# Kernel tuning notes

Measured on AMD Instinct MI355X. Metric: run time of the kernel, lower is better.

Reference implementation:

```python
import jax, jax.numpy as jnp
import numpy as np

K = 8          # num groups / object slots
FC = 256       # fc_size
LAST = 128     # last_fc_size
B = 2048       # batch
M = 1024       # input size
H = 512        # state (hidden) size


def _ln(x, g, b):
    # LayerNorm over last dim, eps matches torch default 1e-5
    mu = jnp.mean(x, axis=-1, keepdims=True)
    var = jnp.mean((x - mu) ** 2, axis=-1, keepdims=True)
    return (x - mu) * jax.lax.rsqrt(var + 1e-5) * g + b


def setup_inputs() -> dict:
    key = jax.random.key(0)
    ks = jax.random.split(key, 10)
    s = 0.05
    d = {
        "x": jax.random.normal(ks[0], (B * K, M), jnp.float32),
        "state": jax.random.normal(ks[1], (B * K, H), jnp.float32),
        # encoder: Linear(H->FC) + LN(FC)
        "enc_w": jax.random.normal(ks[2], (H, FC), jnp.float32) * s,
        "enc_b": jnp.zeros((FC,), jnp.float32),
        "enc_g": jnp.ones((FC,), jnp.float32),
        "enc_bb": jnp.zeros((FC,), jnp.float32),
        # core: Linear(2*FC->FC) + LN(FC)
        "core_w": jax.random.normal(ks[3], (2 * FC, FC), jnp.float32) * s,
        "core_b": jnp.zeros((FC,), jnp.float32),
        "core_g": jnp.ones((FC,), jnp.float32),
        "core_bb": jnp.zeros((FC,), jnp.float32),
        # context: Linear(FC->FC) + LN(FC)
        "ctx_w": jax.random.normal(ks[4], (FC, FC), jnp.float32) * s,
        "ctx_b": jnp.zeros((FC,), jnp.float32),
        "ctx_g": jnp.ones((FC,), jnp.float32),
        "ctx_bb": jnp.zeros((FC,), jnp.float32),
        # attention: Linear(FC->LAST) + LN(LAST) + Tanh + Linear(LAST->1) + Sigmoid
        "att1_w": jax.random.normal(ks[5], (FC, LAST), jnp.float32) * s,
        "att1_b": jnp.zeros((LAST,), jnp.float32),
        "att_g": jnp.ones((LAST,), jnp.float32),
        "att_bb": jnp.zeros((LAST,), jnp.float32),
        "att2_w": jax.random.normal(ks[6], (LAST, 1), jnp.float32) * s,
        "att2_b": jnp.zeros((1,), jnp.float32),
        # out_fc: Linear(FC + FC + M -> FC)
        "out_w": jax.random.normal(ks[7], (FC + FC + M, FC), jnp.float32) * s,
        "out_b": jnp.zeros((FC,), jnp.float32),
    }
    return d


def reference(x, state, enc_w, enc_b, enc_g, enc_bb,
              core_w, core_b, core_g, core_bb,
              ctx_w, ctx_b, ctx_g, ctx_bb,
              att1_w, att1_b, att_g, att_bb, att2_w, att2_b,
              out_w, out_b):
    bk, m = x.shape
    k = K
    b = bk // k
    # 0. encode state: [B*K, H] -> [B*K, FC]
    s1 = jax.nn.relu(_ln(state @ enc_w + enc_b, enc_g, enc_bb))
    h1 = s1.shape[-1]
    s1r = s1.reshape(b, k, h1)
    # focus: K-1 copies of each slot's state  [b, k, k-1, h1]
    fs = jnp.broadcast_to(s1r[:, :, None, :], (b, k, k - 1, h1))
    # context: gather the K-1 other slots' states (replaces torch python loop)
    idx = np.array([[j for j in range(k) if j != i] for i in range(k)])  # [k, k-1]
    cs = s1r[:, idx, :]  # [b, k, k-1, h1]
    concat = jnp.concatenate([fs, cs], axis=-1).reshape(b * k * (k - 1), 2 * h1)
    # core / context MLPs over pairs
    core = jax.nn.relu(_ln(concat @ core_w + core_b, core_g, core_bb))   # [b*k*(k-1), FC]
    ctx = jax.nn.relu(_ln(core @ ctx_w + ctx_b, ctx_g, ctx_bb))          # [b*k*(k-1), FC]
    # attention scalar per pair
    att_h = jnp.tanh(_ln(core @ att1_w + att1_b, att_g, att_bb))
    att = jax.nn.sigmoid(att_h @ att2_w + att2_b)                        # [b*k*(k-1), 1]
    # attention-weighted sum over the K-1 context dim
    h2 = ctx.shape[-1]
    effect = jnp.sum(ctx.reshape(b * k, k - 1, h2) * att.reshape(b * k, k - 1, 1), axis=1)
    # decode: concat encoded state, effect, input -> new state
    total = jnp.concatenate([s1, effect, x], axis=-1)
    new_state = total @ out_w + out_b
    return (new_state, new_state)
```

## Files before the change

kernel.cpp:

```cpp
#include <hip/hip_runtime.h>
#include <stdint.h>

#define FC    256
#define HH    512
#define MX    1024
#define LASTN 128
#define NROW  16384
#define NGRP  2048

typedef unsigned short u16;
typedef __bf16 bf16x8 __attribute__((ext_vector_type(8)));
typedef float  f32x4  __attribute__((ext_vector_type(4)));

__device__ __forceinline__ float red16(float v) {
#pragma unroll
  for (int m = 1; m < 16; m <<= 1) v += __shfl_xor(v, m);
  return v;
}
__device__ __forceinline__ float red16hi(float v) {
#pragma unroll
  for (int m = 4; m < 64; m <<= 1) v += __shfl_xor(v, m);
  return v;
}
__device__ __forceinline__ u16 to_bf16(float f) {
  unsigned u = __float_as_uint(f);
  return (u16)((u + 0x8000u) >> 16);
}
__device__ __forceinline__ float from_bf16(u16 s) {
  return __uint_as_float(((unsigned)s) << 16);
}
__device__ __forceinline__ uint32_t pk2(float a, float b) {
  return (uint32_t)to_bf16(a) | ((uint32_t)to_bf16(b) << 16);
}
__device__ __forceinline__ float tanh_fast(float x) {
  float e = __expf(2.f * x);
  return __fdividef(e - 1.f, e + 1.f);
}
__device__ __forceinline__ float sigmoid_fast(float x) {
  return __fdividef(1.f, 1.f + __expf(-x));
}
__device__ __forceinline__ void glds16(const void* g, void* l) {
  __builtin_amdgcn_global_load_lds(
      (__attribute__((address_space(1))) uint32_t*)g,
      (__attribute__((address_space(3))) uint32_t*)l, 16, 0, 0);
}
__device__ __forceinline__ bf16x8 frag_ld(const u16* p) {
  return __builtin_bit_cast(bf16x8, *(const uint4*)p);
}

__global__ __launch_bounds__(256) void k_prep(
    const float* __restrict__ enc_w, const float* __restrict__ core_w,
    const float* __restrict__ ctx_w, const float* __restrict__ att1_w,
    const float* __restrict__ out_w,
    u16* __restrict__ encT, u16* __restrict__ uvT, u16* __restrict__ ctxT,
    u16* __restrict__ attT, u16* __restrict__ outT)
{
  const int bx = blockIdx.x, tid = threadIdx.x;
  const float* W; u16* D; int NKC, N, local; int uv = 0;
  if (bx < 64)       { W = enc_w;  D = encT; NKC = 16; N = 256; local = bx * 256 + tid; }
  else if (bx < 128) { W = core_w; D = uvT;  NKC = 8;  N = 256; local = (bx-64)*256 + tid; uv = 1; }
  else if (bx < 160) { W = ctx_w;  D = ctxT; NKC = 8;  N = 256; local = (bx-128)*256 + tid; }
  else if (bx < 176) { W = att1_w; D = attT; NKC = 8;  N = 128; local = (bx-160)*256 + tid; }
  else               { W = out_w;  D = outT; NKC = 48; N = 256; local = (bx-176)*256 + tid; }
  const int l  = local & 63;
  const int kc = (local >> 6) % NKC;
  const int u  = (local >> 6) / NKC;
  const int n  = u * 16 + (l & 15);
  const int k0 = kc * 32 + (l >> 4) * 8;
  float f[8];
#pragma unroll
  for (int j = 0; j < 8; ++j) {
    const int k = k0 + j;
    if (uv) f[j] = (n < 256) ? W[(size_t)k * 256 + n] : W[(size_t)(256 + k) * 256 + (n - 256)];
    else    f[j] = W[(size_t)k * N + n];
  }
  uint4 w;
  w.x = pk2(f[0], f[1]); w.y = pk2(f[2], f[3]);
  w.z = pk2(f[4], f[5]); w.w = pk2(f[6], f[7]);
  *(uint4*)&D[(size_t)local * 8] = w;
}

__global__ __launch_bounds__(256) void k_enc(
    const float* __restrict__ state, const u16* __restrict__ encT,
    const float* __restrict__ enc_b, const float* __restrict__ enc_g,
    const float* __restrict__ enc_bb, u16* __restrict__ s1b)
{
  __shared__ __align__(16) u16 smA[2][128 * 8];
  __shared__ __align__(16) u16 smB[2][16 * 64 * 8];
  __shared__ float smP[2][2][16][2];
  const int tid = threadIdx.x, wv = tid >> 6, lane = tid & 63;
  const int cl = lane & 15, quad = lane >> 4;
  const int rb = wv >> 1, cb = wv & 1;
  const int row0 = blockIdx.x * 32;
  f32x4 acc[8];
#pragma unroll
  for (int u = 0; u < 8; ++u) acc[u] = (f32x4){0.f, 0.f, 0.f, 0.f};

  for (int kk = 0; kk < 8; ++kk) {
    __syncthreads();
    {
      const int p = tid >> 7, lu = tid & 127;
      const int kc = kk * 2 + p;
      const int rblk = lu >> 6, ll = lu & 63;
      const float* src = state + (size_t)(row0 + rblk * 16 + (ll & 15)) * HH + kc * 32 + (ll >> 4) * 8;
      float4 a = *(const float4*)src, b = *(const float4*)(src + 4);
      uint4 w; w.x = pk2(a.x, a.y); w.y = pk2(a.z, a.w); w.z = pk2(b.x, b.y); w.w = pk2(b.z, b.w);
      *(uint4*)&smA[p][(size_t)lu * 8] = w;
    }
#pragma unroll
    for (int p = 0; p < 2; ++p)
#pragma unroll
      for (int i = 0; i < 4; ++i) {
        const int u = wv * 4 + i;
        glds16(encT + ((size_t)(u * 16 + kk * 2 + p) * 64 + lane) * 8, &smB[p][u * 512]);
      }
    __syncthreads();
#pragma unroll
    for (int p = 0; p < 2; ++p) {
      bf16x8 af = frag_ld(&smA[p][(rb * 64 + lane) * 8]);
#pragma unroll
      for (int u = 0; u < 8; ++u) {
        bf16x8 bf = frag_ld(&smB[p][((cb * 8 + u) * 64 + lane) * 8]);
        acc[u] = __builtin_amdgcn_mfma_f32_16x16x32_bf16(af, bf, acc[u], 0, 0, 0);
      }
    }
  }
  float bias[8], gg[8], bb[8];
#pragma unroll
  for (int u = 0; u < 8; ++u) {
    const int col = cb * 128 + u * 16 + cl;
    bias[u] = enc_b[col]; gg[u] = enc_g[col]; bb[u] = enc_bb[col];
  }
  float vv[4][8];
#pragma unroll
  for (int r4 = 0; r4 < 4; ++r4) {
    float s = 0.f, sq = 0.f;
#pragma unroll
    for (int u = 0; u < 8; ++u) {
      float v = acc[u][r4] + bias[u];
      vv[r4][u] = v; s += v; sq += v * v;
    }
    s = red16(s); sq = red16(sq);
    if (cl == 0) { smP[cb][rb][quad * 4 + r4][0] = s; smP[cb][rb][quad * 4 + r4][1] = sq; }
  }
  __syncthreads();
#pragma unroll
  for (int r4 = 0; r4 < 4; ++r4) {
    const int rr = quad * 4 + r4;
    const float S  = smP[0][rb][rr][0] + smP[1][rb][rr][0];
    const float SQ = smP[0][rb][rr][1] + smP[1][rb][rr][1];
    const float mu = S * (1.f / 256.f);
    const float rs = rsqrtf(SQ * (1.f / 256.f) - mu * mu + 1e-5f);
    const int row = row0 + rb * 16 + rr;
#pragma unroll
    for (int u = 0; u < 8; ++u) {
      float o = fmaxf((vv[r4][u] - mu) * rs * gg[u] + bb[u], 0.f);
      s1b[(size_t)row * FC + cb * 128 + u * 16 + cl] = to_bf16(o);
    }
  }
}

__global__ __launch_bounds__(256) void k_uv(
    const u16* __restrict__ s1b, const u16* __restrict__ uvT,
    float* __restrict__ UV)
{
  __shared__ __align__(16) u16 smA[2][4 * 64 * 8];
  __shared__ __align__(16) u16 smB[2][8 * 64 * 8];
  const int tid = threadIdx.x, wv = tid >> 6, lane = tid & 63;
  const int cl = lane & 15, quad = lane >> 4;
  const int row0 = blockIdx.x * 64;
  const int nb = blockIdx.y;
  f32x4 acc[8];
#pragma unroll
  for (int u = 0; u < 8; ++u) acc[u] = (f32x4){0.f, 0.f, 0.f, 0.f};

  for (int kk = 0; kk < 4; ++kk) {
    __syncthreads();
#pragma unroll
    for (int p = 0; p < 2; ++p) {
      const int kc = kk * 2 + p;
      glds16(s1b + (size_t)(row0 + wv * 16 + (lane & 15)) * FC + kc * 32 + (lane >> 4) * 8,
             &smA[p][wv * 512]);
#pragma unroll
      for (int i = 0; i < 2; ++i) {
        const int u = wv * 2 + i;
        glds16(uvT + ((size_t)((nb * 8 + u) * 8 + kc) * 64 + lane) * 8, &smB[p][u * 512]);
      }
    }
    __syncthreads();
#pragma unroll
    for (int p = 0; p < 2; ++p) {
      bf16x8 af = frag_ld(&smA[p][(wv * 64 + lane) * 8]);
#pragma unroll
      for (int u = 0; u < 8; ++u) {
        bf16x8 bf = frag_ld(&smB[p][(u * 64 + lane) * 8]);
        acc[u] = __builtin_amdgcn_mfma_f32_16x16x32_bf16(af, bf, acc[u], 0, 0, 0);
      }
    }
  }
#pragma unroll
  for (int r4 = 0; r4 < 4; ++r4) {
    const int row = row0 + wv * 16 + quad * 4 + r4;
#pragma unroll
    for (int u = 0; u < 8; ++u)
      UV[(size_t)row * 512 + nb * 128 + u * 16 + cl] = acc[u][r4];
  }
}

__global__ __launch_bounds__(256, 3) void k_pair(
    const float* __restrict__ UV, const float* __restrict__ core_b,
    const float* __restrict__ core_g, const float* __restrict__ core_bb,
    const u16* __restrict__ ctxT, const float* __restrict__ ctx_b,
    const float* __restrict__ ctx_g, const float* __restrict__ ctx_bb,
    const u16* __restrict__ attT, const float* __restrict__ att1_b,
    const float* __restrict__ att_g, const float* __restrict__ att_bb,
    const float* __restrict__ att2_w, const float* __restrict__ att2_b,
    u16* __restrict__ effb)
{
  __shared__ __align__(16) u16 smA[2048 * 8];
  __shared__ __align__(16) u16 smX[16 * 64 * 8];
  __shared__ float att_s[64];
  float* smUV = (float*)smX;
  u16*   smB  = smX;
  const int g = blockIdx.x;
  const int tid = threadIdx.x, wv = tid >> 6, lane = tid & 63;
  const int cl = lane & 15, quad = lane >> 4;
  const int aswz = ((lane >> 5) & 1) << 2;

#pragma unroll
  for (int i = 0; i < 4; ++i) {
    const int r = wv * 4 + i;
    const int row = g * 8 + (r & 7);
    const int half = r >> 3;
    glds16(UV + (size_t)row * 512 + half * 256 + lane * 4, &smUV[r * 256]);
  }
#pragma unroll
  for (int i = 0; i < 8; ++i)
    *(uint4*)&smA[(size_t)(tid + i * 256) * 8] = (uint4){0u, 0u, 0u, 0u};
  __syncthreads();

  {
    const int s4  = lane & 3;
    const int g16 = lane >> 2;
    const int c0  = g16 * 16;
    float4 CB[4], CG[4], CBB[4];
#pragma unroll
    for (int q = 0; q < 4; ++q) {
      const int cq = c0 + ((q ^ s4) << 2);
      CB[q]  = *(const float4*)&core_b[cq];
      CG[q]  = *(const float4*)&core_g[cq];
      CBB[q] = *(const float4*)&core_bb[cq];
    }
#pragma unroll
    for (int it = 0; it < 4; ++it) {
      const int p = it * 16 + wv * 4 + s4;
      if (p < 56) {
        const int i = p / 7, t = p - i * 7;
        const int j = t + (t >= i ? 1 : 0);
        const float* uA = &smUV[i * 256 + c0];
        const float* vB = &smUV[(8 + j) * 256 + c0];
        float v[16];
        float s = 0.f, sq = 0.f;
#pragma unroll
        for (int q = 0; q < 4; ++q) {
          const int qo = (q ^ s4) << 2;
          float4 ua = *(const float4*)(uA + qo);
          float4 vb = *(const float4*)(vB + qo);
          float x0 = ua.x + vb.x + CB[q].x, x1 = ua.y + vb.y + CB[q].y;
          float x2 = ua.z + vb.z + CB[q].z, x3 = ua.w + vb.w + CB[q].w;
          v[q*4+0] = x0; v[q*4+1] = x1; v[q*4+2] = x2; v[q*4+3] = x3;
          s += x0 + x1 + x2 + x3;
          sq += x0*x0 + x1*x1 + x2*x2 + x3*x3;
        }
        s = red16hi(s); sq = red16hi(sq);
        const float mu = s * (1.f / 256.f);
        const float rs = rsqrtf(sq * (1.f / 256.f) - mu * mu + 1e-5f);
#pragma unroll
        for (int q = 0; q < 4; ++q) {
          v[q*4+0] = fmaxf((v[q*4+0] - mu) * rs * CG[q].x + CBB[q].x, 0.f);
          v[q*4+1] = fmaxf((v[q*4+1] - mu) * rs * CG[q].y + CBB[q].y, 0.f);
          v[q*4+2] = fmaxf((v[q*4+2] - mu) * rs * CG[q].z + CBB[q].z, 0.f);
          v[q*4+3] = fmaxf((v[q*4+3] - mu) * rs * CG[q].w + CBB[q].w, 0.f);
        }
#pragma unroll
        for (int q = 0; q < 4; ++q) {
          const int lg = q ^ s4;
          const int ks = (g16 * 2 + (lg >> 1)) & 3;
          int slot = ((p >> 4) * 8 + (g16 >> 1)) * 64 + (p & 15) + 16 * ks;
          slot ^= ((slot >> 5) & 1) << 2;
          uint2 w;
          w.x = pk2(v[q*4+0], v[q*4+1]);
          w.y = pk2(v[q*4+2], v[q*4+3]);
          *(uint2*)&smA[(size_t)slot * 8 + (lg & 1) * 4] = w;
        }
      }
    }
  }
  __syncthreads();

  f32x4 accT[8];
#pragma unroll
  for (int t = 0; t < 8; ++t) accT[t] = (f32x4){0.f, 0.f, 0.f, 0.f};
#pragma unroll 2
  for (int kc = 0; kc < 8; ++kc) {
    uint4 attf[8];
#pragma unroll
    for (int q = 0; q < 8; ++q)
      attf[q] = *(const uint4*)(attT + ((size_t)(q * 8 + kc) * 64 + lane) * 8);
    bf16x8 af = frag_ld(&smA[(size_t)((((wv * 8 + kc) * 64) + lane) ^ aswz) * 8]);
#pragma unroll
    for (int q = 0; q < 8; ++q) {
      bf16x8 bf = __builtin_bit_cast(bf16x8, attf[q]);
      accT[q] = __builtin_amdgcn_mfma_f32_16x16x32_bf16(af, bf, accT[q], 0, 0, 0);
    }
  }

  {
    float ab[8], ag[8], abb[8], aw[8];
#pragma unroll
    for (int t = 0; t < 8; ++t) {
      const int col = t * 16 + cl;
      ab[t] = att1_b[col]; ag[t] = att_g[col]; abb[t] = att_bb[col]; aw[t] = att2_w[col];
    }
    const float b2 = att2_b[0];
#pragma unroll
    for (int r4 = 0; r4 < 4; ++r4) {
      float v[8], s = 0.f, sq = 0.f;
#pragma unroll
      for (int t = 0; t < 8; ++t) {
        v[t] = accT[t][r4] + ab[t];
        s += v[t]; sq += v[t] * v[t];
      }
      s = red16(s); sq = red16(sq);
      const float mu = s * (1.f / 128.f);
      const float rs = rsqrtf(sq * (1.f / 128.f) - mu * mu + 1e-5f);
      float d = 0.f;
#pragma unroll
      for (int t = 0; t < 8; ++t) {
        float h = tanh_fast((v[t] - mu) * rs * ag[t] + abb[t]);
        d = fmaf(h, aw[t], d);
      }
      d = red16(d);
      if (cl == 0) {
        const int r = wv * 16 + quad * 4 + r4;
        if (r < 56) att_s[r] = sigmoid_fast(d + b2);
      }
    }
  }

  f32x4 accC[16];
#pragma unroll
  for (int t = 0; t < 16; ++t) accC[t] = (f32x4){0.f, 0.f, 0.f, 0.f};
  for (int kc = 0; kc < 8; ++kc) {
    if (kc) __syncthreads();
#pragma unroll
    for (int i = 0; i < 4; ++i) {
      const int q = wv * 4 + i;
      glds16(ctxT + ((size_t)(q * 8 + kc) * 64 + lane) * 8, &smB[q * 512]);
    }
    __syncthreads();
    bf16x8 af = frag_ld(&smA[(size_t)((((wv * 8 + kc) * 64) + lane) ^ aswz) * 8]);
#pragma unroll
    for (int q = 0; q < 16; ++q) {
      bf16x8 bf = frag_ld(&smB[(q * 64 + lane) * 8]);
      accC[q] = __builtin_amdgcn_mfma_f32_16x16x32_bf16(af, bf, accC[q], 0, 0, 0);
    }
  }
  __syncthreads();

  u16* smS = smA;
  {
    float cb[16], cg[16], cbb[16];
#pragma unroll
    for (int t = 0; t < 16; ++t) {
      const int col = t * 16 + cl;
      cb[t] = ctx_b[col]; cg[t] = ctx_g[col]; cbb[t] = ctx_bb[col];
    }
#pragma unroll
    for (int r4 = 0; r4 < 4; ++r4) {
      float v[16], s = 0.f, sq = 0.f;
#pragma unroll
      for (int t = 0; t < 16; ++t) {
        v[t] = accC[t][r4] + cb[t];
        s += v[t]; sq += v[t] * v[t];
      }
      s = red16(s); sq = red16(sq);
      const float mu = s * (1.f / 256.f);
      const float rs = rsqrtf(sq * (1.f / 256.f) - mu * mu + 1e-5f);
      const int r = wv * 16 + quad * 4 + r4;
      if (r < 56) {
        const float ap = att_s[r];
#pragma unroll
        for (int t = 0; t < 16; ++t) {
          const int col = t * 16 + cl;
          float o = fmaxf((v[t] - mu) * rs * cg[t] + cbb[t], 0.f) * ap;
          smS[r * 264 + col] = to_bf16(o);
        }
      }
    }
  }
  __syncthreads();

  const int c = tid;
#pragma unroll
  for (int i = 0; i < 8; ++i) {
    float s = 0.f;
#pragma unroll
    for (int t2 = 0; t2 < 7; ++t2) s += from_bf16(smS[(i * 7 + t2) * 264 + c]);
    effb[(size_t)(g * 8 + i) * FC + c] = to_bf16(s);
  }
}

__global__ __launch_bounds__(256) void k_out(
    const u16* __restrict__ s1b, const u16* __restrict__ effb,
    const float* __restrict__ x, const u16* __restrict__ outT,
    const float* __restrict__ out_b, float* __restrict__ out, int dup)
{
  __shared__ __align__(16) u16 smA[2][4 * 64 * 8];
  __shared__ __align__(16) u16 smB[2][8 * 64 * 8];
  const int tid = threadIdx.x, wv = tid >> 6, lane = tid & 63;
  const int cl = lane & 15, quad = lane >> 4;
  const int row0 = blockIdx.x * 64;
  const int nb = blockIdx.y;
  f32x4 acc[8];
#pragma unroll
  for (int u = 0; u < 8; ++u) acc[u] = (f32x4){0.f, 0.f, 0.f, 0.f};

  for (int kk = 0; kk < 24; ++kk) {
    const int kc0 = kk * 2;
    __syncthreads();
    if (kc0 < 16) {
#pragma unroll
      for (int p = 0; p < 2; ++p) {
        const int kc = kc0 + p;
        const u16* base = (kc < 8) ? s1b : effb;
        const int kof = (kc & 7) * 32;
        glds16(base + (size_t)(row0 + wv * 16 + (lane & 15)) * FC + kof + (lane >> 4) * 8,
               &smA[p][wv * 512]);
      }
    } else {
      const int t = tid >> 6, ll = tid & 63;
      const float* src0 = x + (size_t)(row0 + t * 16 + (ll & 15)) * MX + (ll >> 4) * 8;
#pragma unroll
      for (int p = 0; p < 2; ++p) {
        const float* src = src0 + (kc0 + p - 16) * 32;
        float4 a = *(const float4*)src, b = *(const float4*)(src + 4);
        uint4 w; w.x = pk2(a.x, a.y); w.y = pk2(a.z, a.w); w.z = pk2(b.x, b.y); w.w = pk2(b.z, b.w);
        *(uint4*)&smA[p][(size_t)tid * 8] = w;
      }
    }
#pragma unroll
    for (int p = 0; p < 2; ++p)
#pragma unroll
      for (int i = 0; i < 2; ++i) {
        const int u = wv * 2 + i;
        glds16(outT + ((size_t)((nb * 8 + u) * 48 + kc0 + p) * 64 + lane) * 8, &smB[p][u * 512]);
      }
    __syncthreads();
#pragma unroll
    for (int p = 0; p < 2; ++p) {
      bf16x8 af = frag_ld(&smA[p][(wv * 64 + lane) * 8]);
#pragma unroll
      for (int u = 0; u < 8; ++u) {
        bf16x8 bf = frag_ld(&smB[p][(u * 64 + lane) * 8]);
        acc[u] = __builtin_amdgcn_mfma_f32_16x16x32_bf16(af, bf, acc[u], 0, 0, 0);
      }
    }
  }
  float bias[8];
#pragma unroll
  for (int u = 0; u < 8; ++u) bias[u] = out_b[nb * 128 + u * 16 + cl];
#pragma unroll
  for (int r4 = 0; r4 < 4; ++r4) {
    const int row = row0 + wv * 16 + quad * 4 + r4;
#pragma unroll
    for (int u = 0; u < 8; ++u) {
      const float o = acc[u][r4] + bias[u];
      const size_t off = (size_t)row * FC + nb * 128 + u * 16 + cl;
      out[off] = o;
      if (dup) out[(size_t)NROW * FC + off] = o;
    }
  }
}

extern "C" void kernel_launch(void* const* d_in, const int* in_sizes, int n_in,
                              void* d_out, int out_size, void* d_ws, size_t ws_size,
                              hipStream_t stream) {
  const float* x      = (const float*)d_in[0];
  const float* state  = (const float*)d_in[1];
  const float* enc_w  = (const float*)d_in[2];
  const float* enc_b  = (const float*)d_in[3];
  const float* enc_g  = (const float*)d_in[4];
  const float* enc_bb = (const float*)d_in[5];
  const float* core_w = (const float*)d_in[6];
  const float* core_b = (const float*)d_in[7];
  const float* core_g = (const float*)d_in[8];
  const float* core_bb= (const float*)d_in[9];
  const float* ctx_w  = (const float*)d_in[10];
  const float* ctx_b  = (const float*)d_in[11];
  const float* ctx_g  = (const float*)d_in[12];
  const float* ctx_bb = (const float*)d_in[13];
  const float* att1_w = (const float*)d_in[14];
  const float* att1_b = (const float*)d_in[15];
  const float* att_g  = (const float*)d_in[16];
  const float* att_bb = (const float*)d_in[17];
  const float* att2_w = (const float*)d_in[18];
  const float* att2_b = (const float*)d_in[19];
  const float* out_w  = (const float*)d_in[20];
  const float* out_b  = (const float*)d_in[21];

  char* ws = (char*)d_ws;
  float* UV  = (float*)ws;
  u16* s1b   = (u16*)(ws + 33554432);
  u16* effb  = (u16*)(ws + 41943040);
  u16* encT  = (u16*)(ws + 50331648);
  u16* uvT   = (u16*)(ws + 50593792);
  u16* ctxT  = (u16*)(ws + 50855936);
  u16* attT  = (u16*)(ws + 50987008);
  u16* outT  = (u16*)(ws + 51052544);
  float* out = (float*)d_out;
  const int dup = (out_size >= 2 * NROW * FC) ? 1 : 0;

  k_prep<<<dim3(368), 256, 0, stream>>>(enc_w, core_w, ctx_w, att1_w, out_w,
                                        encT, uvT, ctxT, attT, outT);
  k_enc<<<dim3(NROW / 32), 256, 0, stream>>>(state, encT, enc_b, enc_g, enc_bb, s1b);
  k_uv <<<dim3(NROW / 64, 4), 256, 0, stream>>>(s1b, uvT, UV);
  k_pair<<<dim3(NGRP), 256, 0, stream>>>(UV, core_b, core_g, core_bb,
                                         ctxT, ctx_b, ctx_g, ctx_bb,
                                         attT, att1_b, att_g, att_bb,
                                         att2_w, att2_b, effb);
  k_out<<<dim3(NROW / 64, 2), 256, 0, stream>>>(s1b, effb, x, outT, out_b, out, dup);
}
```

Before: 290.3 us.

## Split ctx GEMM by output columns per wave with register-held weights

```diff
diff --git a/kernel.cpp b/kernel.cpp
--- a/kernel.cpp
+++ b/kernel.cpp
@@ -220,8 +220,8 @@
   __shared__ __align__(16) u16 smA[2048 * 8];
   __shared__ __align__(16) u16 smX[16 * 64 * 8];
   __shared__ float att_s[64];
-  float* smUV = (float*)smX;
-  u16*   smB  = smX;
+  float* smUV  = (float*)smX;
+  float* partf = (float*)smX;
   const int g = blockIdx.x;
   const int tid = threadIdx.x, wv = tid >> 6, lane = tid & 63;
   const int cl = lane & 15, quad = lane >> 4;
@@ -351,54 +351,73 @@
   f32x4 accC[16];
 #pragma unroll
   for (int t = 0; t < 16; ++t) accC[t] = (f32x4){0.f, 0.f, 0.f, 0.f};
+#pragma unroll 2
   for (int kc = 0; kc < 8; ++kc) {
-    if (kc) __syncthreads();
-#pragma unroll
-    for (int i = 0; i < 4; ++i) {
-      const int q = wv * 4 + i;
-      glds16(ctxT + ((size_t)(q * 8 + kc) * 64 + lane) * 8, &smB[q * 512]);
-    }
-    __syncthreads();
-    bf16x8 af = frag_ld(&smA[(size_t)((((wv * 8 + kc) * 64) + lane) ^ aswz) * 8]);
-#pragma unroll
-    for (int q = 0; q < 16; ++q) {
-      bf16x8 bf = frag_ld(&smB[(q * 64 + lane) * 8]);
-      accC[q] = __builtin_amdgcn_mfma_f32_16x16x32_bf16(af, bf, accC[q], 0, 0, 0);
-    }
-  }
+    uint4 cf[4];
+#pragma unroll
+    for (int i = 0; i < 4; ++i)
+      cf[i] = *(const uint4*)(ctxT + ((size_t)((wv * 4 + i) * 8 + kc) * 64 + lane) * 8);
+    bf16x8 af[4];
+#pragma unroll
+    for (int rt = 0; rt < 4; ++rt)
+      af[rt] = frag_ld(&smA[(size_t)((((rt * 8 + kc) * 64) + lane) ^ aswz) * 8]);
+#pragma unroll
+    for (int rt = 0; rt < 4; ++rt)
+#pragma unroll
+      for (int i = 0; i < 4; ++i) {
+        bf16x8 bf = __builtin_bit_cast(bf16x8, cf[i]);
+        accC[rt * 4 + i] = __builtin_amdgcn_mfma_f32_16x16x32_bf16(af[rt], bf, accC[rt * 4 + i], 0, 0, 0);
+      }
+  }
+
+  float cbw[4], cgw[4], cbbw[4];
+#pragma unroll
+  for (int i = 0; i < 4; ++i) {
+    const int col = (wv * 4 + i) * 16 + cl;
+    cbw[i] = ctx_b[col]; cgw[i] = ctx_g[col]; cbbw[i] = ctx_bb[col];
+  }
+#pragma unroll
+  for (int rt = 0; rt < 4; ++rt)
+#pragma unroll
+    for (int r4 = 0; r4 < 4; ++r4) {
+      float s = 0.f, sq = 0.f;
+#pragma unroll
+      for (int i = 0; i < 4; ++i) {
+        const float v = accC[rt * 4 + i][r4] + cbw[i];
+        s += v; sq += v * v;
+      }
+      s = red16(s); sq = red16(sq);
+      if (cl == 0) {
+        const int r = rt * 16 + quad * 4 + r4;
+        partf[(wv * 64 + r) * 2 + 0] = s;
+        partf[(wv * 64 + r) * 2 + 1] = sq;
+      }
+    }
   __syncthreads();
 
   u16* smS = smA;
-  {
-    float cb[16], cg[16], cbb[16];
-#pragma unroll
-    for (int t = 0; t < 16; ++t) {
-      const int col = t * 16 + cl;
-      cb[t] = ctx_b[col]; cg[t] = ctx_g[col]; cbb[t] = ctx_bb[col];
-    }
+#pragma unroll
+  for (int rt = 0; rt < 4; ++rt)
 #pragma unroll
     for (int r4 = 0; r4 < 4; ++r4) {
-      float v[16], s = 0.f, sq = 0.f;
-#pragma unroll
-      for (int t = 0; t < 16; ++t) {
-        v[t] = accC[t][r4] + cb[t];
-        s += v[t]; sq += v[t] * v[t];
-      }
-      s = red16(s); sq = red16(sq);
-      const float mu = s * (1.f / 256.f);
-      const float rs = rsqrtf(sq * (1.f / 256.f) - mu * mu + 1e-5f);
-      const int r = wv * 16 + quad * 4 + r4;
+      const int r = rt * 16 + quad * 4 + r4;
       if (r < 56) {
+        const float S  = partf[(0 * 64 + r) * 2 + 0] + partf[(1 * 64 + r) * 2 + 0]
+                       + partf[(2 * 64 + r) * 2 + 0] + partf[(3 * 64 + r) * 2 + 0];
+        const float SQ = partf[(0 * 64 + r) * 2 + 1] + partf[(1 * 64 + r) * 2 + 1]
+                       + partf[(2 * 64 + r) * 2 + 1] + partf[(3 * 64 + r) * 2 + 1];
+        const float mu = S * (1.f / 256.f);
+        const float rs = rsqrtf(SQ * (1.f / 256.f) - mu * mu + 1e-5f);
         const float ap = att_s[r];
 #pragma unroll
-        for (int t = 0; t < 16; ++t) {
-          const int col = t * 16 + cl;
-          float o = fmaxf((v[t] - mu) * rs * cg[t] + cbb[t], 0.f) * ap;
+        for (int i = 0; i < 4; ++i) {
+          const int col = (wv * 4 + i) * 16 + cl;
+          const float v = accC[rt * 4 + i][r4] + cbw[i];
+          const float o = fmaxf((v - mu) * rs * cgw[i] + cbbw[i], 0.f) * ap;
           smS[r * 264 + col] = to_bf16(o);
         }
       }
     }
-  }
   __syncthreads();
 
   const int c = tid;
```

Result: no change. 292.9 us (+0.9%).
